# Optimization experiments

Hardware: AMD Instinct MI355X
Metric: run time of the kernel (lower is better)

The kernel has to match this reference:

```python
import jax, jax.numpy as jnp
import numpy as np

N = 32768   # 'a' nodes
K = 8       # incoming edges per node (regular graph)
K2 = K // 2
E = N * K   # edges, stored as reverse pairs (2i, 2i+1)
D = 300     # hid_dim
H = 4       # attention heads
DEPTH = 3


def _build_graph():
    i = np.arange(N)
    src = np.empty(E, np.int64)
    mail = np.empty((N, K), np.int64)
    for d in range(1, K2 + 1):
        base = 2 * (i * K2 + (d - 1))
        src[base] = i                 # edge i -> (i+d)%N
        src[base + 1] = (i + d) % N   # reverse edge (i+d)%N -> i
        # incoming edges of node v: ((v-d)->v) and ((v+d)->v)
        mail[:, 2 * (d - 1)] = 2 * (((i - d) % N) * K2 + (d - 1))
        mail[:, 2 * (d - 1) + 1] = 2 * (i * K2 + (d - 1)) + 1
    return src, mail


def setup_inputs() -> dict:
    key = jax.random.key(0)
    ks = jax.random.split(key, 12)
    s = 1.0 / np.sqrt(D)
    src, mail = _build_graph()
    return {
        'f': jax.random.normal(ks[0], (N, D), jnp.float32),
        'x': jax.random.normal(ks[1], (E, D), jnp.float32),
        'mail_idx': jnp.asarray(mail),
        'src_idx': jnp.asarray(src),
        'Wq': jax.random.normal(ks[2], (D, D), jnp.float32) * s,
        'bq': jnp.zeros((D,), jnp.float32),
        'Wk': jax.random.normal(ks[3], (D, D), jnp.float32) * s,
        'bk': jnp.zeros((D,), jnp.float32),
        'Wv': jax.random.normal(ks[4], (D, D), jnp.float32) * s,
        'bv': jnp.zeros((D,), jnp.float32),
        'Wo': jax.random.normal(ks[5], (D, D), jnp.float32) * s,
        'bo': jnp.zeros((D,), jnp.float32),
        'Wmp': jax.random.normal(ks[6], (DEPTH - 1, D, D), jnp.float32) * s,
        'bmp': jnp.zeros((DEPTH - 1, D), jnp.float32),
        'Wlast': jax.random.normal(ks[7], (3 * D, D), jnp.float32) * s,
        'blast': jnp.zeros((D,), jnp.float32),
    }


def _mha(q_in, k_in, v_in, Wq, bq, Wk, bk, Wv, bv, Wo, bo):
    # q_in: [N,1,D], k_in/v_in: [N,K,D]  (per-node neighborhood attention)
    dk = D // H
    q = (q_in @ Wq + bq).reshape(N, 1, H, dk).transpose(0, 2, 1, 3)
    k = (k_in @ Wk + bk).reshape(N, -1, H, dk).transpose(0, 2, 1, 3)
    v = (v_in @ Wv + bv).reshape(N, -1, H, dk).transpose(0, 2, 1, 3)
    scores = jnp.einsum('nhqd,nhkd->nhqk', q, k) / jnp.sqrt(jnp.float32(dk))
    p = jax.nn.softmax(scores, axis=-1)
    o = jnp.einsum('nhqk,nhkd->nhqd', p, v).transpose(0, 2, 1, 3).reshape(N, 1, D)
    return o @ Wo + bo


def reference(f, x, mail_idx, src_idx, Wq, bq, Wk, bk, Wv, bv, Wo, bo,
              Wmp, bmp, Wlast, blast):
    rev = jnp.arange(E) ^ 1  # reverse_edge: swap within consecutive pairs
    f_h = f              # init_node: f_h = f.clone()
    h = x                # init_edge: h = x.clone()
    for i in range(DEPTH - 1):
        mail = h[mail_idx]                    # copy_e mailbox [N,K,D]
        feat = f_h[:, None, :]                # [N,1,D]
        # add_attn: attn(feat, mail, mail + feat)
        f_h = _mha(feat, mail, mail + feat,
                   Wq, bq, Wk, bk, Wv, bv, Wo, bo)[:, 0, :]
        rev_h = h[rev]                        # paired reverse-edge feature
        m = f_h[src_idx] - rev_h              # del_reverse_message
        h = jax.nn.relu(x + m @ Wmp[i] + bmp[i])  # update_edge
    # final node update: Linear(cat([sum(mailbox h), f_h, f]))
    mail_sum = jnp.sum(h[mail_idx], axis=1)   # [N,D]
    f_final = jnp.concatenate([mail_sum, f_h, f], axis=1) @ Wlast + blast
    return f_final
```

## Files before the change

### kernel.cpp

```cpp
#include <hip/hip_runtime.h>

typedef unsigned short u16;
typedef unsigned int u32;
typedef __bf16 bf16x8 __attribute__((ext_vector_type(8)));
typedef float f32x4 __attribute__((ext_vector_type(4)));

#define N_NODES 32768
#define E_EDGES 262144
#define BQ_U16 26240
#define S75 0.11547005383792515f

__device__ __forceinline__ float b2f(u16 u) {
    union { u32 u; float f; } x; x.u = ((u32)u) << 16; return x.f;
}
__device__ __forceinline__ u16 f2b(float f) {
    union { float f; u32 u; } x; x.f = f;
    u32 r = x.u + 0x7FFF + ((x.u >> 16) & 1);
    return (u16)(r >> 16);
}
__device__ __forceinline__ u32 bsub2(u32 a, u32 b) {
    float lo = b2f((u16)(a & 0xFFFF)) - b2f((u16)(b & 0xFFFF));
    float hi = b2f((u16)(a >> 16))    - b2f((u16)(b >> 16));
    return (u32)f2b(lo) | ((u32)f2b(hi) << 16);
}

#define GLOAD16(g, l) \
    __builtin_amdgcn_global_load_lds((const __attribute__((address_space(1))) u32*)(g), \
                                     (__attribute__((address_space(3))) u32*)(l), 16, 0, 0)

__global__ void convT_k(const float* __restrict__ src, int R, int C,
                        u16* __restrict__ dst, int KP_, long total) {
    long id = (long)blockIdx.x * blockDim.x + threadIdx.x;
    if (id >= total) return;
    int n = (int)(id / KP_), k = (int)(id % KP_);
    dst[id] = (k < R && n < C) ? f2b(src[(long)k * C + n]) : (u16)0;
}

__global__ void convTq_k(const float* __restrict__ src, u16* __restrict__ dst) {
    int id = blockIdx.x * 256 + threadIdx.x;
    if (id >= 4 * BQ_U16) return;
    int q = id / BQ_U16, rem = id % BQ_U16;
    int r = rem / 328, c = rem % 328;
    int n = q * 80 + r;
    dst[id] = (c < 300 && n < 300) ? f2b(src[(long)c * 300 + n]) : (u16)0;
}

__global__ void wqkq_k(const float* __restrict__ Wq, const float* __restrict__ Wk,
                       u16* __restrict__ dst) {
    int id = blockIdx.x * 256 + threadIdx.x;
    if (id >= 16 * BQ_U16) return;
    int q = id / BQ_U16, rem = id % BQ_U16;
    int r = rem / 328, c = rem % 328;
    int h = q >> 2;
    int cc = (q & 3) * 80 + r;
    float acc = 0.f;
    if (c < 300 && cc < 300) {
        const float* wq = Wq + (long)c * 300 + 75 * h;
        const float* wk = Wk + (long)cc * 300 + 75 * h;
        for (int d = 0; d < 75; ++d) acc += wq[d] * wk[d];
        acc *= S75;
    }
    dst[id] = f2b(acc);
}

__global__ void bqk_k(const float* __restrict__ bq, const float* __restrict__ Wk,
                      float* __restrict__ dst) {
    int n = blockIdx.x * 256 + threadIdx.x;
    if (n >= 1280) return;
    int h = n / 320, cc = n % 320;
    float acc = 0.f;
    if (cc < 300) {
        const float* b = bq + 75 * h;
        const float* wk = Wk + (long)cc * 300 + 75 * h;
        for (int d = 0; d < 75; ++d) acc += b[d] * wk[d];
        acc *= S75;
    }
    dst[n] = acc;
}

__global__ void ucat_k(const float* __restrict__ Wv, const float* __restrict__ Wo,
                       u16* __restrict__ dst) {
    long id = (long)blockIdx.x * 256 + threadIdx.x;
    if (id >= 320L * 1600) return;
    int n = (int)(id / 1600), k = (int)(id % 1600);
    float acc = 0.f;
    if (n < 300) {
        if (k < 1280) {
            int h = k / 320, a = k % 320;
            if (a < 300) {
                const float* wv = Wv + (long)a * 300 + 75 * h;
                const float* wo = Wo + (long)(75 * h) * 300 + n;
                for (int d = 0; d < 75; ++d) acc += wv[d] * wo[(long)d * 300];
            }
        } else {
            int a = k - 1280;
            if (a < 300) {
                const float* wv = Wv + (long)a * 300;
                const float* wo = Wo + n;
                for (int d = 0; d < 300; ++d) acc += wv[d] * wo[(long)d * 300];
            }
        }
    }
    dst[id] = f2b(acc);
}

__global__ void bvo_k(const float* __restrict__ bv, const float* __restrict__ Wo,
                      const float* __restrict__ bo, float* __restrict__ dst) {
    int n = blockIdx.x * 256 + threadIdx.x;
    if (n >= 320) return;
    float acc = 0.f;
    if (n < 300) {
        for (int d = 0; d < 300; ++d) acc += bv[d] * Wo[(long)d * 300 + n];
        acc += bo[n];
    }
    dst[n] = acc;
}

__global__ void padconv_k(const float* __restrict__ src, int C,
                          u16* __restrict__ dst, int CP,
                          u16* __restrict__ dst2, int CP2, long total) {
    long id = (long)blockIdx.x * blockDim.x + threadIdx.x;
    if (id >= total) return;
    int cw = CP >> 3;
    long row = id / cw;
    int c8 = (int)(id % cw) * 8;
    u32 w[4];
    #pragma unroll
    for (int p = 0; p < 4; ++p) {
        int c0 = c8 + 2 * p, c1 = c0 + 1;
        u16 lo = (c0 < C) ? f2b(src[row * C + c0]) : (u16)0;
        u16 hi = (c1 < C) ? f2b(src[row * C + c1]) : (u16)0;
        w[p] = (u32)lo | ((u32)hi << 16);
    }
    u32* d = (u32*)(dst + row * CP + c8);
    d[0] = w[0]; d[1] = w[1]; d[2] = w[2]; d[3] = w[3];
    if (dst2) {
        u32* d2 = (u32*)(dst2 + row * CP2 + c8);
        d2[0] = w[0]; d2[1] = w[1]; d2[2] = w[2]; d2[3] = w[3];
    }
}

#define TCOMP(KB, APTR) do { \
    bf16x8 av_[2], bb_[5]; \
    _Pragma("unroll") for (int fr = 0; fr < 2; ++fr) \
        av_[fr] = *(const bf16x8*)&(APTR)[ar0 + fr * 512]; \
    _Pragma("unroll") for (int fc = 0; fc < 5; ++fc) \
        bb_[fc] = *(const bf16x8*)&Bs[br0 + fc * 5248 + (KB) * 32]; \
    __builtin_amdgcn_s_setprio(1); \
    _Pragma("unroll") for (int fr = 0; fr < 2; ++fr) \
        _Pragma("unroll") for (int fc = 0; fc < 5; ++fc) \
            acc[fr][fc] = __builtin_amdgcn_mfma_f32_16x16x32_bf16(bb_[fc], av_[fr], acc[fr][fc], 0, 0, 0); \
    __builtin_amdgcn_s_setprio(0); \
} while (0)

__global__ __launch_bounds__(256, 2) void qgemm_k(
    const u16* __restrict__ A, const u16* __restrict__ Bswz,
    const float* __restrict__ bias, u16* __restrict__ outB)
{
    __shared__ __attribute__((aligned(16))) u16 Bs[80 * 328];
    __shared__ __attribute__((aligned(16))) u16 As3[3][128 * 32];
    const int tid = threadIdx.x;
    const int wf = tid >> 6, lane = tid & 63;
    const int tl = lane & 15, thi = lane >> 4;
    const int bid = blockIdx.x;
    const int gid = (bid & 7) * ((int)gridDim.x >> 3) + (bid >> 3);
    const long m0 = (long)(gid >> 4) * 128;
    const int q = gid & 15;
    const int n0 = q * 80;
    const int wf_u = __builtin_amdgcn_readfirstlane(wf);
    const u16* Bsrc = Bswz + q * BQ_U16;

    #pragma unroll
    for (int i = 0; i < 13; ++i) {
        int t = i * 256 + tid;
        if (t < 3280)
            GLOAD16(Bsrc + (long)t * 8, &Bs[(i * 256 + wf_u * 64) * 8]);
    }
    const int r1 = tid >> 2;
    const int g1 = (tid & 3) ^ ((r1 >> 1) & 3);
    const u16* gA0 = A + (m0 + r1) * 320L + g1 * 8;
    const u16* gA1 = A + (m0 + 64 + r1) * 320L + g1 * 8;

#define ESTAGE(KB) { \
    GLOAD16(gA0 + (KB) * 32, &As3[(KB) % 3][wf_u * 512]); \
    GLOAD16(gA1 + (KB) * 32, &As3[(KB) % 3][2048 + wf_u * 512]); }

    ESTAGE(0); ESTAGE(1);

    f32x4 acc[2][5];
    #pragma unroll
    for (int i = 0; i < 2; ++i)
        #pragma unroll
        for (int j = 0; j < 5; ++j) acc[i][j] = (f32x4)(0.f);
    const int ar0 = (wf * 32 + tl) * 32 + (thi ^ ((tl >> 1) & 3)) * 8;
    const int br0 = tl * 328 + thi * 8;

#define ESTEP(KB, VN) { \
    asm volatile("s_waitcnt vmcnt(" #VN ")" ::: "memory"); \
    __builtin_amdgcn_s_barrier(); \
    __builtin_amdgcn_sched_barrier(0); \
    if ((KB) + 2 < 10) ESTAGE((KB) + 2); \
    TCOMP(KB, (&As3[(KB) % 3][0])); }

    ESTEP(0, 2) ESTEP(1, 2) ESTEP(2, 2) ESTEP(3, 2) ESTEP(4, 2)
    ESTEP(5, 2) ESTEP(6, 2) ESTEP(7, 2) ESTEP(8, 2) ESTEP(9, 0)
#undef ESTEP
#undef ESTAGE

    #pragma unroll
    for (int fr = 0; fr < 2; ++fr) {
        const long row = m0 + wf * 32 + fr * 16 + tl;
        #pragma unroll
        for (int fc = 0; fc < 5; ++fc) {
            const int c0 = n0 + fc * 16 + thi * 4;
            f32x4 v = acc[fr][fc];
            const float4 bs = *(const float4*)&bias[c0];
            v[0] += bs.x; v[1] += bs.y; v[2] += bs.z; v[3] += bs.w;
            uint2 p;
            p.x = (u32)f2b(v[0]) | ((u32)f2b(v[1]) << 16);
            p.y = (u32)f2b(v[2]) | ((u32)f2b(v[3]) << 16);
            *(uint2*)&outB[row * 1280 + c0] = p;
        }
    }
}

__global__ __launch_bounds__(256) void attn2_k(
    const u16* __restrict__ qg, const u16* __restrict__ hcur,
    const int* __restrict__ mail, u16* __restrict__ wideA)
{
    const int tid = threadIdx.x;
    const long n = (long)blockIdx.x * 4 + (tid >> 6);
    const int lane = tid & 63;
    const bool act = lane < 40;
    const int ll = act ? lane : 39;

    int idx[8];
    #pragma unroll
    for (int j = 0; j < 8; ++j) idx[j] = mail[n * 8 + j];
    uint4 hr[8];
    #pragma unroll
    for (int j = 0; j < 8; ++j)
        hr[j] = *(const uint4*)&hcur[(long)idx[j] * 320 + ll * 8];
    uint4 qv[4];
    #pragma unroll
    for (int h = 0; h < 4; ++h)
        qv[h] = *(const uint4*)&qg[n * 1280 + h * 320 + ll * 8];
    if (!act) {
        #pragma unroll
        for (int j = 0; j < 8; ++j) hr[j] = make_uint4(0, 0, 0, 0);
    }

    float qf[4][8];
    #pragma unroll
    for (int h = 0; h < 4; ++h) {
        const u32 w[4] = {qv[h].x, qv[h].y, qv[h].z, qv[h].w};
        #pragma unroll
        for (int p = 0; p < 4; ++p) {
            qf[h][2 * p]     = b2f((u16)(w[p] & 0xFFFF));
            qf[h][2 * p + 1] = b2f((u16)(w[p] >> 16));
        }
    }

    float s[4][8];
    #pragma unroll
    for (int j = 0; j < 8; ++j) {
        float hf[8];
        const u32 w[4] = {hr[j].x, hr[j].y, hr[j].z, hr[j].w};
        #pragma unroll
        for (int p = 0; p < 4; ++p) {
            hf[2 * p]     = b2f((u16)(w[p] & 0xFFFF));
            hf[2 * p + 1] = b2f((u16)(w[p] >> 16));
        }
        #pragma unroll
        for (int h = 0; h < 4; ++h) {
            float d = 0.f;
            #pragma unroll
            for (int m = 0; m < 8; ++m) d += qf[h][m] * hf[m];
            d += __shfl_xor(d, 32, 64);
            d += __shfl_xor(d, 16, 64);
            d += __shfl_xor(d, 8, 64);
            d += __shfl_xor(d, 4, 64);
            d += __shfl_xor(d, 2, 64);
            d += __shfl_xor(d, 1, 64);
            s[h][j] = d;
        }
    }

    float p_[4][8];
    #pragma unroll
    for (int h = 0; h < 4; ++h) {
        float mx = s[h][0];
        #pragma unroll
        for (int j = 1; j < 8; ++j) mx = fmaxf(mx, s[h][j]);
        float sum = 0.f;
        #pragma unroll
        for (int j = 0; j < 8; ++j) { p_[h][j] = __expf(s[h][j] - mx); sum += p_[h][j]; }
        const float inv = 1.f / sum;
        #pragma unroll
        for (int j = 0; j < 8; ++j) p_[h][j] *= inv;
    }

    float y[4][8];
    #pragma unroll
    for (int h = 0; h < 4; ++h)
        #pragma unroll
        for (int m = 0; m < 8; ++m) y[h][m] = 0.f;
    #pragma unroll
    for (int j = 0; j < 8; ++j) {
        float hf[8];
        const u32 w[4] = {hr[j].x, hr[j].y, hr[j].z, hr[j].w};
        #pragma unroll
        for (int p = 0; p < 4; ++p) {
            hf[2 * p]     = b2f((u16)(w[p] & 0xFFFF));
            hf[2 * p + 1] = b2f((u16)(w[p] >> 16));
        }
        #pragma unroll
        for (int h = 0; h < 4; ++h)
            #pragma unroll
            for (int m = 0; m < 8; ++m) y[h][m] += p_[h][j] * hf[m];
    }
    if (act) {
        #pragma unroll
        for (int h = 0; h < 4; ++h) {
            uint4 o;
            o.x = (u32)f2b(y[h][0]) | ((u32)f2b(y[h][1]) << 16);
            o.y = (u32)f2b(y[h][2]) | ((u32)f2b(y[h][3]) << 16);
            o.z = (u32)f2b(y[h][4]) | ((u32)f2b(y[h][5]) << 16);
            o.w = (u32)f2b(y[h][6]) | ((u32)f2b(y[h][7]) << 16);
            *(uint4*)&wideA[n * 1600 + h * 320 + lane * 8] = o;
        }
    }
}

__global__ __launch_bounds__(256, 2) void egemmmb_k(
    const u16* __restrict__ fhb, const u16* __restrict__ hcur,
    const u16* __restrict__ hx, const int* __restrict__ srcidx,
    const u16* __restrict__ Bswz, const float* __restrict__ bias,
    u16* __restrict__ outB)
{
    __shared__ __attribute__((aligned(16))) u16 Bs[80 * 328];
    const int tid = threadIdx.x;
    const int wf = tid >> 6, lane = tid & 63;
    const int tl = lane & 15, thi = lane >> 4;
    const int bid = blockIdx.x;
    const int gid = (bid & 7) * ((int)gridDim.x >> 3) + (bid >> 3);
    const long m0 = (long)(gid >> 2) * 64;
    const int q = gid & 3;
    const int n0 = q * 80;
    const int wf_u = __builtin_amdgcn_readfirstlane(wf);
    const u16* Bsrc = Bswz + q * BQ_U16;

    #pragma unroll
    for (int i = 0; i < 13; ++i) {
        int t = i * 256 + tid;
        if (t < 3280)
            GLOAD16(Bsrc + (long)t * 8, &Bs[(i * 256 + wf_u * 64) * 8]);
    }
    __builtin_amdgcn_sched_barrier(0);

    const long e = m0 + wf * 16 + tl;
    const u16* pF = fhb + (long)srcidx[e] * 320 + thi * 8;
    const u16* pH = hcur + (e ^ 1) * 320 + thi * 8;

    uint4 Fa0, Fa1, Ha0, Ha1, Fb0, Fb1, Hb0, Hb1, Fc0, Fc1, Hc0, Hc1;

#define MLD(KB, F0, F1, H0, H1) { \
    F0 = *(const uint4*)(pF + (KB) * 64);      F1 = *(const uint4*)(pF + (KB) * 64 + 32); \
    H0 = *(const uint4*)(pH + (KB) * 64);      H1 = *(const uint4*)(pH + (KB) * 64 + 32); }

    MLD(0, Fa0, Fa1, Ha0, Ha1);
    MLD(1, Fb0, Fb1, Hb0, Hb1);
    __builtin_amdgcn_sched_barrier(0);
    asm volatile("s_waitcnt vmcnt(8)" ::: "memory");
    __builtin_amdgcn_s_barrier();
    __builtin_amdgcn_sched_barrier(0);

    f32x4 acc[5];
    #pragma unroll
    for (int j = 0; j < 5; ++j) acc[j] = (f32x4)(0.f);
    const int br0 = tl * 328 + thi * 8;

#define GC(KB, F0, F1, H0, H1) { \
    uint4 o0_, o1_; \
    o0_.x = bsub2(F0.x, H0.x); o0_.y = bsub2(F0.y, H0.y); \
    o0_.z = bsub2(F0.z, H0.z); o0_.w = bsub2(F0.w, H0.w); \
    o1_.x = bsub2(F1.x, H1.x); o1_.y = bsub2(F1.y, H1.y); \
    o1_.z = bsub2(F1.z, H1.z); o1_.w = bsub2(F1.w, H1.w); \
    bf16x8 av0_ = *(const bf16x8*)&o0_; \
    bf16x8 av1_ = *(const bf16x8*)&o1_; \
    __builtin_amdgcn_s_setprio(1); \
    _Pragma("unroll") for (int fc = 0; fc < 5; ++fc) { \
        const u16* br_ = &Bs[br0 + fc * 5248 + (KB) * 64]; \
        bf16x8 b0_ = *(const bf16x8*)&br_[0]; \
        acc[fc] = __builtin_amdgcn_mfma_f32_16x16x32_bf16(b0_, av0_, acc[fc], 0, 0, 0); \
        bf16x8 b1_ = *(const bf16x8*)&br_[32]; \
        acc[fc] = __builtin_amdgcn_mfma_f32_16x16x32_bf16(b1_, av1_, acc[fc], 0, 0, 0); } \
    __builtin_amdgcn_s_setprio(0); }

    MLD(2, Fc0, Fc1, Hc0, Hc1); GC(0, Fa0, Fa1, Ha0, Ha1);
    MLD(3, Fa0, Fa1, Ha0, Ha1); GC(1, Fb0, Fb1, Hb0, Hb1);
    MLD(4, Fb0, Fb1, Hb0, Hb1); GC(2, Fc0, Fc1, Hc0, Hc1);
    GC(3, Fa0, Fa1, Ha0, Ha1);
    GC(4, Fb0, Fb1, Hb0, Hb1);
#undef GC
#undef MLD

    const long row = m0 + wf * 16 + tl;
    #pragma unroll
    for (int fc = 0; fc < 5; ++fc) {
        const int c0 = n0 + fc * 16 + thi * 4;
        f32x4 v = acc[fc];
        if (c0 < 300) {
            const float4 bs = *(const float4*)&bias[c0];
            v[0] += bs.x; v[1] += bs.y; v[2] += bs.z; v[3] += bs.w;
        }
        {
            const ushort4 xv = *(const ushort4*)&hx[row * 320 + c0];
            v[0] += b2f(xv.x); v[1] += b2f(xv.y); v[2] += b2f(xv.z); v[3] += b2f(xv.w);
        }
        v[0] = fmaxf(v[0], 0.f); v[1] = fmaxf(v[1], 0.f);
        v[2] = fmaxf(v[2], 0.f); v[3] = fmaxf(v[3], 0.f);
        uint2 p;
        p.x = (u32)f2b(v[0]) | ((u32)f2b(v[1]) << 16);
        p.y = (u32)f2b(v[2]) | ((u32)f2b(v[3]) << 16);
        *(uint2*)&outB[row * 320 + c0] = p;
    }
}

#define LOADB(bq, kt1) { const long ko_ = (long)(kt1) << 6; \
    _Pragma("unroll") for (int fc = 0; fc < 5; ++fc) \
      _Pragma("unroll") for (int ks = 0; ks < 2; ++ks) \
        bq[fc][ks] = *(const bf16x8*)(gBw + (long)fc * 16 * KP + ko_ + ks * 32); }

#define READA(lkt) { \
    _Pragma("unroll") for (int fr = 0; fr < 4; ++fr) \
      _Pragma("unroll") for (int ks = 0; ks < 2; ++ks) \
        a[fr][ks] = *(const bf16x8*)&As[(fr * 16 + tl) * 320 + ((((lkt) * 8 + ks * 4 + thi) ^ sx) * 8)]; }

#define DOMFMA(bq) { _Pragma("unroll") for (int fr = 0; fr < 4; ++fr) \
    _Pragma("unroll") for (int fc = 0; fc < 5; ++fc) \
      _Pragma("unroll") for (int ks = 0; ks < 2; ++ks) \
        acc[fr][fc] = __builtin_amdgcn_mfma_f32_16x16x32_bf16(bq[fc][ks], a[fr][ks], acc[fr][fc], 0, 0, 0); }

template<int KP>
__global__ __launch_bounds__(256, 2) void gemm_k(
    const u16* __restrict__ A,
    const u16* __restrict__ BT,
    const float* __restrict__ bias,
    float* __restrict__ outF, int ostride, int ocols,
    u16* __restrict__ outB1, long strideB1,
    u16* __restrict__ outB2, long strideB2)
{
    __shared__ u16 As[64 * 320];
    const int tid = threadIdx.x;
    const int w = tid >> 6, lane = tid & 63;
    const int tl = lane & 15, thi = lane >> 4;
    const int sx = tl & 7;
    const long m0 = (long)blockIdx.x * 64;
    const int w_u = __builtin_amdgcn_readfirstlane(w);

    const u16* gBw = BT + ((long)(w * 80 + tl)) * KP + thi * 8;

    f32x4 acc[4][5];
    #pragma unroll
    for (int i = 0; i < 4; ++i)
        #pragma unroll
        for (int j = 0; j < 5; ++j) acc[i][j] = (f32x4)(0.f);

    constexpr int NCH = KP / 320;
    constexpr int NST = KP >> 6;
    bf16x8 bA[5][2], bB[5][2], a[4][2];

    #pragma unroll
    for (int kb = 0; kb < NCH; ++kb) {
        if (kb) __syncthreads();
        #pragma unroll
        for (int i = 0; i < 10; ++i) {
            const int c = i * 256 + w_u * 64 + lane;
            const int r = c / 40, s = c - r * 40;
            GLOAD16(A + (m0 + r) * (long)KP + kb * 320 + ((s ^ (r & 7)) * 8),
                    &As[(i * 256 + w_u * 64) * 8]);
        }
        if (kb == 0) LOADB(bA, 0);
        __syncthreads();
        #pragma unroll
        for (int lkt = 0; lkt < 5; ++lkt) {
            const int kt = kb * 5 + lkt;
            if (kt + 1 < NST) {
                if (kt & 1) { LOADB(bA, kt + 1); } else { LOADB(bB, kt + 1); }
            }
            READA(lkt);
            if (kt & 1) { DOMFMA(bB); } else { DOMFMA(bA); }
        }
    }

    #pragma unroll
    for (int fr = 0; fr < 4; ++fr) {
        const long row = m0 + fr * 16 + tl;
        #pragma unroll
        for (int fc = 0; fc < 5; ++fc) {
            const int c0 = w * 80 + fc * 16 + thi * 4;
            f32x4 v = acc[fr][fc];
            if (bias && c0 < 300) {
                const float4 bs = *(const float4*)&bias[c0];
                v[0] += bs.x; v[1] += bs.y; v[2] += bs.z; v[3] += bs.w;
            }
            if (outF && c0 < ocols)
                *(float4*)&outF[row * (long)ostride + c0] = make_float4(v[0], v[1], v[2], v[3]);
            if (outB1 || outB2) {
                uint2 p;
                p.x = (u32)f2b(v[0]) | ((u32)f2b(v[1]) << 16);
                p.y = (u32)f2b(v[2]) | ((u32)f2b(v[3]) << 16);
                if (outB1) *(uint2*)&outB1[row * strideB1 + c0] = p;
                if (outB2) *(uint2*)&outB2[row * strideB2 + c0] = p;
            }
        }
    }
}

__global__ __launch_bounds__(256) void concat_k(
    const u16* __restrict__ hb, const u16* __restrict__ fhb,
    const float* __restrict__ f, const int* __restrict__ mail,
    u16* __restrict__ Acat)
{
    const long n = blockIdx.x;
    int m[8];
    #pragma unroll
    for (int j = 0; j < 8; ++j) m[j] = mail[n * 8 + j];
    for (int c = threadIdx.x; c < 960; c += 256) {
        float v;
        if (c < 300) {
            float s = 0.f;
            #pragma unroll
            for (int j = 0; j < 8; ++j) s += b2f(hb[(long)m[j] * 320 + c]);
            v = s;
        } else if (c < 600) v = b2f(fhb[n * 320 + (c - 300)]);
        else if (c < 900) v = f[n * 300 + (c - 600)];
        else v = 0.f;
        Acat[n * 960 + c] = f2b(v);
    }
}

extern "C" void kernel_launch(void* const* d_in, const int* in_sizes, int n_in,
                              void* d_out, int out_size, void* d_ws, size_t ws_size,
                              hipStream_t stream)
{
    const int N = N_NODES, E = E_EDGES;
    const float* f    = (const float*)d_in[0];
    const float* x    = (const float*)d_in[1];
    const int*   mail = (const int*)d_in[2];
    const int*   srcx = (const int*)d_in[3];
    const float* Wq = (const float*)d_in[4];   const float* bq = (const float*)d_in[5];
    const float* Wk = (const float*)d_in[6];
    const float* Wv = (const float*)d_in[8];   const float* bv = (const float*)d_in[9];
    const float* Wo = (const float*)d_in[10];  const float* bo = (const float*)d_in[11];
    const float* Wmp = (const float*)d_in[12]; const float* bmp = (const float*)d_in[13];
    const float* Wlast = (const float*)d_in[14]; const float* blast = (const float*)d_in[15];
    float* out = (float*)d_out;

    char* ws = (char*)d_ws;
    size_t off = 0;
    auto alloc = [&](size_t b) -> void* {
        void* p = ws + off; off += (b + 255) & ~(size_t)255; return p;
    };
    u16* hb    = (u16*)alloc((size_t)E * 320 * 2);
    u16* hb2   = (u16*)alloc((size_t)E * 320 * 2);
    u16* qgb   = (u16*)alloc((size_t)N * 1280 * 2);
    u16* wideA = (u16*)alloc((size_t)N * 1600 * 2);
    u16* fhb   = (u16*)alloc((size_t)N * 320 * 2);
    u16* Acat  = (u16*)alloc((size_t)N * 960 * 2);
    u16* WqkS  = (u16*)alloc((size_t)16 * BQ_U16 * 2);
    u16* Wm0S  = (u16*)alloc((size_t)4 * BQ_U16 * 2);
    u16* Wm1S  = (u16*)alloc((size_t)4 * BQ_U16 * 2);
    u16* UcatT = (u16*)alloc((size_t)320 * 1600 * 2);
    u16* WcatB = (u16*)alloc((size_t)960 * 320 * 2);
    float* bqkF = (float*)alloc(1280 * 4);
    float* bvoF = (float*)alloc(320 * 4);

    {
        wqkq_k<<<(16 * BQ_U16 + 255) / 256, 256, 0, stream>>>(Wq, Wk, WqkS);
        bqk_k<<<5, 256, 0, stream>>>(bq, Wk, bqkF);
        ucat_k<<<(int)((320L * 1600 + 255) / 256), 256, 0, stream>>>(Wv, Wo, UcatT);
        bvo_k<<<2, 256, 0, stream>>>(bv, Wo, bo, bvoF);
        int blks = (4 * BQ_U16 + 255) / 256;
        convTq_k<<<blks, 256, 0, stream>>>(Wmp, Wm0S);
        convTq_k<<<blks, 256, 0, stream>>>(Wmp + 90000, Wm1S);
        long totc = (long)320 * 960;
        convT_k<<<(int)((totc + 255) / 256), 256, 0, stream>>>(Wlast, 900, 300, WcatB, 960, totc);
    }
    {
        long totE = (long)E * 40;
        padconv_k<<<(int)((totE + 255) / 256), 256, 0, stream>>>(x, 300, hb, 320, nullptr, 0, totE);
        long totN = (long)N * 40;
        padconv_k<<<(int)((totN + 255) / 256), 256, 0, stream>>>(f, 300, fhb, 320, wideA + 1280, 1600, totN);
    }

    const int GQG = (N / 128) * 16;
    const int GE4 = (E / 64) * 4;

    for (int it = 0; it < 2; ++it) {
        const u16* WmS = it ? Wm1S : Wm0S;
        const float* bmpi = bmp + it * 300;
        const u16* hcur = it ? hb2 : hb;
        u16* hnxt = it ? hb : hb2;
        qgemm_k<<<GQG, 256, 0, stream>>>(fhb, WqkS, bqkF, qgb);
        attn2_k<<<N / 4, 256, 0, stream>>>(qgb, hcur, mail, wideA);
        gemm_k<1600><<<N / 64, 256, 0, stream>>>(wideA, UcatT, bvoF,
                                                 nullptr, 0, 0, fhb, 320, wideA + 1280, 1600);
        egemmmb_k<<<GE4, 256, 0, stream>>>(fhb, hcur, hb, srcx, WmS, bmpi, hnxt);
    }

    concat_k<<<N, 256, 0, stream>>>(hb, fhb, f, mail, Acat);
    gemm_k<960><<<N / 64, 256, 0, stream>>>(Acat, WcatB, blast, out, 300, 300,
                                            nullptr, 0, nullptr, 0);
}
```

Baseline: 1.384 ms.

## Split edge GEMM into two MFMA accumulators and use 512-thread blocks

The per-element bf16 subtraction of gathered node and reverse-edge features is removed. Each operand now feeds its own MFMA accumulator, and the two results are subtracted in fp32 in the epilogue. Blocks grow to 512 threads covering 128 edge rows, so each weight tile staged in LDS is shared by twice as many rows. This avoids the scalar convert/subtract/round work but doubles the MFMA count and accumulator registers, and the launch bounds now ask for 4 blocks of 512 threads per CU.

```diff
diff --git a/kernel.cpp b/kernel.cpp
--- a/kernel.cpp
+++ b/kernel.cpp
@@ -17,11 +17,6 @@
     union { float f; u32 u; } x; x.f = f;
     u32 r = x.u + 0x7FFF + ((x.u >> 16) & 1);
     return (u16)(r >> 16);
-}
-__device__ __forceinline__ u32 bsub2(u32 a, u32 b) {
-    float lo = b2f((u16)(a & 0xFFFF)) - b2f((u16)(b & 0xFFFF));
-    float hi = b2f((u16)(a >> 16))    - b2f((u16)(b >> 16));
-    return (u32)f2b(lo) | ((u32)f2b(hi) << 16);
 }
 
 #define GLOAD16(g, l) \
@@ -332,7 +327,7 @@
     }
 }
 
-__global__ __launch_bounds__(256, 2) void egemmmb_k(
+__global__ __launch_bounds__(512, 4) void egemmmb_k(
     const u16* __restrict__ fhb, const u16* __restrict__ hcur,
     const u16* __restrict__ hx, const int* __restrict__ srcidx,
     const u16* __restrict__ Bswz, const float* __restrict__ bias,
@@ -344,17 +339,17 @@
     const int tl = lane & 15, thi = lane >> 4;
     const int bid = blockIdx.x;
     const int gid = (bid & 7) * ((int)gridDim.x >> 3) + (bid >> 3);
-    const long m0 = (long)(gid >> 2) * 64;
+    const long m0 = (long)(gid >> 2) * 128;
     const int q = gid & 3;
     const int n0 = q * 80;
     const int wf_u = __builtin_amdgcn_readfirstlane(wf);
     const u16* Bsrc = Bswz + q * BQ_U16;
 
     #pragma unroll
-    for (int i = 0; i < 13; ++i) {
-        int t = i * 256 + tid;
+    for (int i = 0; i < 7; ++i) {
+        int t = i * 512 + tid;
         if (t < 3280)
-            GLOAD16(Bsrc + (long)t * 8, &Bs[(i * 256 + wf_u * 64) * 8]);
+            GLOAD16(Bsrc + (long)t * 8, &Bs[(i * 512 + wf_u * 64) * 8]);
     }
     __builtin_amdgcn_sched_barrier(0);
 
@@ -375,26 +370,25 @@
     __builtin_amdgcn_s_barrier();
     __builtin_amdgcn_sched_barrier(0);
 
-    f32x4 acc[5];
-    #pragma unroll
-    for (int j = 0; j < 5; ++j) acc[j] = (f32x4)(0.f);
+    f32x4 accF[5], accH[5];
+    #pragma unroll
+    for (int j = 0; j < 5; ++j) { accF[j] = (f32x4)(0.f); accH[j] = (f32x4)(0.f); }
     const int br0 = tl * 328 + thi * 8;
 
 #define GC(KB, F0, F1, H0, H1) { \
-    uint4 o0_, o1_; \
-    o0_.x = bsub2(F0.x, H0.x); o0_.y = bsub2(F0.y, H0.y); \
-    o0_.z = bsub2(F0.z, H0.z); o0_.w = bsub2(F0.w, H0.w); \
-    o1_.x = bsub2(F1.x, H1.x); o1_.y = bsub2(F1.y, H1.y); \
-    o1_.z = bsub2(F1.z, H1.z); o1_.w = bsub2(F1.w, H1.w); \
-    bf16x8 av0_ = *(const bf16x8*)&o0_; \
-    bf16x8 av1_ = *(const bf16x8*)&o1_; \
+    bf16x8 af0_ = *(const bf16x8*)&F0; \
+    bf16x8 af1_ = *(const bf16x8*)&F1; \
+    bf16x8 ah0_ = *(const bf16x8*)&H0; \
+    bf16x8 ah1_ = *(const bf16x8*)&H1; \
     __builtin_amdgcn_s_setprio(1); \
     _Pragma("unroll") for (int fc = 0; fc < 5; ++fc) { \
         const u16* br_ = &Bs[br0 + fc * 5248 + (KB) * 64]; \
         bf16x8 b0_ = *(const bf16x8*)&br_[0]; \
-        acc[fc] = __builtin_amdgcn_mfma_f32_16x16x32_bf16(b0_, av0_, acc[fc], 0, 0, 0); \
+        accF[fc] = __builtin_amdgcn_mfma_f32_16x16x32_bf16(b0_, af0_, accF[fc], 0, 0, 0); \
+        accH[fc] = __builtin_amdgcn_mfma_f32_16x16x32_bf16(b0_, ah0_, accH[fc], 0, 0, 0); \
         bf16x8 b1_ = *(const bf16x8*)&br_[32]; \
-        acc[fc] = __builtin_amdgcn_mfma_f32_16x16x32_bf16(b1_, av1_, acc[fc], 0, 0, 0); } \
+        accF[fc] = __builtin_amdgcn_mfma_f32_16x16x32_bf16(b1_, af1_, accF[fc], 0, 0, 0); \
+        accH[fc] = __builtin_amdgcn_mfma_f32_16x16x32_bf16(b1_, ah1_, accH[fc], 0, 0, 0); } \
     __builtin_amdgcn_s_setprio(0); }
 
     MLD(2, Fc0, Fc1, Hc0, Hc1); GC(0, Fa0, Fa1, Ha0, Ha1);
@@ -409,7 +403,11 @@
     #pragma unroll
     for (int fc = 0; fc < 5; ++fc) {
         const int c0 = n0 + fc * 16 + thi * 4;
-        f32x4 v = acc[fc];
+        f32x4 v;
+        v[0] = accF[fc][0] - accH[fc][0];
+        v[1] = accF[fc][1] - accH[fc][1];
+        v[2] = accF[fc][2] - accH[fc][2];
+        v[3] = accF[fc][3] - accH[fc][3];
         if (c0 < 300) {
             const float4 bs = *(const float4*)&bias[c0];
             v[0] += bs.x; v[1] += bs.y; v[2] += bs.z; v[3] += bs.w;
@@ -596,18 +594,18 @@
     }
 
     const int GQG = (N / 128) * 16;
-    const int GE4 = (E / 64) * 4;
+    const int GE2 = (E / 128) * 4;
 
     for (int it = 0; it < 2; ++it) {
+        const float* bmpi = bmp + it * 300;
         const u16* WmS = it ? Wm1S : Wm0S;
-        const float* bmpi = bmp + it * 300;
         const u16* hcur = it ? hb2 : hb;
         u16* hnxt = it ? hb : hb2;
         qgemm_k<<<GQG, 256, 0, stream>>>(fhb, WqkS, bqkF, qgb);
         attn2_k<<<N / 4, 256, 0, stream>>>(qgb, hcur, mail, wideA);
         gemm_k<1600><<<N / 64, 256, 0, stream>>>(wideA, UcatT, bvoF,
                                                  nullptr, 0, 0, fhb, 320, wideA + 1280, 1600);
-        egemmmb_k<<<GE4, 256, 0, stream>>>(fhb, hcur, hb, srcx, WmS, bmpi, hnxt);
+        egemmmb_k<<<GE2, 512, 0, stream>>>(fhb, hcur, hb, srcx, WmS, bmpi, hnxt);
     }
 
     concat_k<<<N, 256, 0, stream>>>(hb, fhb, f, mail, Acat);
```

Result: faster. 1.339 ms (-3.2%).
